# Performance work log

Measured on AMD Instinct MI355X. Metric: run time of the kernel, lower is better.

The kernel has to match this reference:

```python
import jax, jax.numpy as jnp
import numpy as np

B, S, DIM = 2, 2048, 2048
H, DK, DR, DC, DCP, DV = 16, 128, 64, 512, 1024, 128


def setup_inputs() -> dict:
    key = jax.random.key(0)
    ks = jax.random.split(key, 8)
    s = 0.02  # weight init scale
    return {
        "x": jax.random.normal(ks[0], (B, S, DIM), jnp.float32),
        "W_c": jax.random.normal(ks[1], (DIM, DC), jnp.float32) * s,
        "W_c_prime": jax.random.normal(ks[2], (DIM, DCP), jnp.float32) * s,
        "W_qc": jax.random.normal(ks[3], (H, DCP, DK), jnp.float32) * s,
        "W_qr": jax.random.normal(ks[4], (H, DCP, DR), jnp.float32) * s,
        "W_kc": jax.random.normal(ks[5], (H, DC, DK), jnp.float32) * s,
        "W_kr": jax.random.normal(ks[6], (DIM, DR), jnp.float32) * s,
        "W_v": jax.random.normal(ks[7], (H, DC, DV), jnp.float32) * s,
    }


def reference(x, W_c, W_c_prime, W_qc, W_qr, W_kc, W_kr, W_v):
    # Latent compressions
    c = x @ W_c                 # [B,S,DC]  compressed KV latent
    cp = x @ W_c_prime          # [B,S,DCP] compressed Q latent
    # Per-head projections, vectorized over heads
    q_c = jnp.einsum('bsc,hck->bhsk', cp, W_qc)   # [B,H,S,DK]
    q_r = jnp.einsum('bsc,hcr->bhsr', cp, W_qr)   # [B,H,S,DR]
    k_c = jnp.einsum('bsc,hck->bhsk', c, W_kc)    # [B,H,S,DK]
    k_r = x @ W_kr                                 # [B,S,DR] shared across heads
    q = jnp.concatenate([q_c, q_r], axis=-1)                               # [B,H,S,DK+DR]
    k = jnp.concatenate([k_c, jnp.broadcast_to(k_r[:, None], (B, H, S, DR))], axis=-1)
    scale = 1.0 / np.sqrt(DK + DR)
    scores = jnp.einsum('bhsd,bhtd->bhst', q, k) * scale                   # [B,H,S,S]
    causal = jnp.tril(jnp.ones((S, S), dtype=bool))
    scores = jnp.where(causal, scores, -jnp.inf)
    probs = jax.nn.softmax(scores.astype(jnp.float32), axis=-1).astype(q.dtype)
    v = jnp.einsum('bsc,hcv->bhsv', c, W_v)                                # [B,H,S,DV]
    out = jnp.einsum('bhst,bhtv->bhsv', probs, v)                          # [B,H,S,DV]
    return out.transpose(0, 2, 1, 3).reshape(B, S, H * DV)                 # concat heads
```

## Files before the change

kernel.cpp:

```cpp
#include <hip/hip_runtime.h>
#include <stdint.h>

typedef __bf16 bf16;
typedef __bf16 bfx8 __attribute__((ext_vector_type(8)));
typedef __bf16 bfx4 __attribute__((ext_vector_type(4)));
typedef float floatx4 __attribute__((ext_vector_type(4)));

#define B_ 2
#define S_ 2048
#define DIM_ 2048
#define H_ 16
#define DK_ 128
#define DR_ 64
#define DC_ 512
#define DCP_ 1024
#define DV_ 128
#define DQK_ 192

#define MASK_VAL (-30000.0f)
#define C1_ 0.10411754f

__global__ void k_cast(const float* __restrict__ in, bf16* __restrict__ out) {
    size_t i = ((size_t)blockIdx.x * 256 + threadIdx.x) * 8;
    float4 a = *(const float4*)(in + i);
    float4 b = *(const float4*)(in + i + 4);
    bfx8 r;
    r[0] = (bf16)a.x; r[1] = (bf16)a.y; r[2] = (bf16)a.z; r[3] = (bf16)a.w;
    r[4] = (bf16)b.x; r[5] = (bf16)b.y; r[6] = (bf16)b.z; r[7] = (bf16)b.w;
    *(bfx8*)(out + i) = r;
}

__global__ void k_transpose(const float* __restrict__ in, bf16* __restrict__ out,
                            int K, int N) {
    __shared__ float tile[32][33];
    int h = blockIdx.z;
    int n0 = blockIdx.x * 32, k0 = blockIdx.y * 32;
    const float* ip = in + (size_t)h * K * N;
    bf16* op = out + (size_t)h * K * N;
    int tx = threadIdx.x & 31, ty = threadIdx.x >> 5;
#pragma unroll
    for (int i = 0; i < 32; i += 8)
        tile[ty + i][tx] = ip[(size_t)(k0 + ty + i) * N + (n0 + tx)];
    __syncthreads();
#pragma unroll
    for (int i = 0; i < 32; i += 8)
        op[(size_t)(n0 + ty + i) * K + (k0 + tx)] = (bf16)tile[tx][ty + i];
}

__device__ __forceinline__ void gld16(const bf16* g, bf16* l) {
    __builtin_amdgcn_global_load_lds(
        (const __attribute__((address_space(1))) void*)g,
        (__attribute__((address_space(3))) void*)l, 16, 0, 0);
}

__device__ __forceinline__ bfx8 frag_ld(const bf16* lds, int row, int quad) {
    int pb = quad ^ ((row >> 1) & 3);
    return *(const bfx8*)(lds + row * 32 + pb * 8);
}

__device__ __forceinline__ void gemm_core(const bf16* __restrict__ A,
                                          const bf16* __restrict__ Bt,
                                          int K, int rowlimB,
                                          floatx4 acc[4][4],
                                          bf16* A_lds, bf16* B_lds) {
    int tid = threadIdx.x, wave = tid >> 6, lane = tid & 63;
    int l15 = lane & 15, quad = lane >> 4;
    int wm = (wave & 1) * 64, wn = (wave >> 1) * 64;
    int ch0 = wave * 2, ch1 = wave * 2 + 1;
    int r0 = ch0 * 16 + (lane >> 2), r1 = ch1 * 16 + (lane >> 2);
    int kb0 = (lane & 3) ^ ((r0 >> 1) & 3), kb1 = (lane & 3) ^ ((r1 >> 1) & 3);
    int rb0 = r0 <= rowlimB ? r0 : rowlimB;
    int rb1 = r1 <= rowlimB ? r1 : rowlimB;
    const bf16* a0 = A + (size_t)r0 * K + kb0 * 8;
    const bf16* a1 = A + (size_t)r1 * K + kb1 * 8;
    const bf16* b0 = Bt + (size_t)rb0 * K + kb0 * 8;
    const bf16* b1 = Bt + (size_t)rb1 * K + kb1 * 8;
    bf16* da0 = A_lds + ch0 * 512;
    bf16* da1 = A_lds + ch1 * 512;
    bf16* db0 = B_lds + ch0 * 512;
    bf16* db1 = B_lds + ch1 * 512;
    for (int k0 = 0; k0 < K; k0 += 32) {
        __syncthreads();
        gld16(a0 + k0, da0);
        gld16(a1 + k0, da1);
        gld16(b0 + k0, db0);
        gld16(b1 + k0, db1);
        __syncthreads();
        bfx8 a[4], b[4];
#pragma unroll
        for (int t = 0; t < 4; ++t) a[t] = frag_ld(A_lds, wm + t * 16 + l15, quad);
#pragma unroll
        for (int t = 0; t < 4; ++t) b[t] = frag_ld(B_lds, wn + t * 16 + l15, quad);
#pragma unroll
        for (int mt = 0; mt < 4; ++mt)
#pragma unroll
            for (int nt = 0; nt < 4; ++nt)
                acc[mt][nt] = __builtin_amdgcn_mfma_f32_16x16x32_bf16(
                    a[mt], b[nt], acc[mt][nt], 0, 0, 0);
    }
}

__global__ __launch_bounds__(256, 3) void k_gemm1(
    const bf16* __restrict__ xb, const bf16* __restrict__ Wt_c,
    const bf16* __restrict__ Wt_cp, const bf16* __restrict__ Wt_kr,
    bf16* __restrict__ c_ws, bf16* __restrict__ cp_ws, bf16* __restrict__ kr_ws) {
    __shared__ __attribute__((aligned(16))) bf16 A_lds[128 * 32];
    __shared__ __attribute__((aligned(16))) bf16 B_lds[128 * 32];
    int bx = blockIdx.x, by = blockIdx.y;
    const bf16* Bt; bf16* outp; int ldc, col0, rowlim;
    if (bx < 4)       { Bt = Wt_c  + (size_t)bx * 128 * DIM_;       outp = c_ws;  ldc = DC_;  col0 = bx * 128;       rowlim = 127; }
    else if (bx < 12) { Bt = Wt_cp + (size_t)(bx - 4) * 128 * DIM_; outp = cp_ws; ldc = DCP_; col0 = (bx - 4) * 128; rowlim = 127; }
    else              { Bt = Wt_kr;                                  outp = kr_ws; ldc = DR_;  col0 = 0;              rowlim = 63;  }
    floatx4 acc[4][4];
#pragma unroll
    for (int i = 0; i < 4; ++i)
#pragma unroll
        for (int j = 0; j < 4; ++j) acc[i][j] = (floatx4){0.f, 0.f, 0.f, 0.f};
    gemm_core(xb + (size_t)by * 128 * DIM_, Bt, DIM_, rowlim, acc, A_lds, B_lds);
    int tid = threadIdx.x, wave = tid >> 6, lane = tid & 63;
    int l15 = lane & 15, quad = lane >> 4;
    int wm = (wave & 1) * 64, wn = (wave >> 1) * 64;
#pragma unroll
    for (int mt = 0; mt < 4; ++mt)
#pragma unroll
        for (int nt = 0; nt < 4; ++nt) {
            int n = wn + nt * 16 + l15;
            if (n > rowlim) continue;
#pragma unroll
            for (int r = 0; r < 4; ++r) {
                int m = by * 128 + wm + mt * 16 + quad * 4 + r;
                outp[(size_t)m * ldc + col0 + n] = (bf16)acc[mt][nt][r];
            }
        }
}

__global__ __launch_bounds__(256, 3) void k_gemm2(
    const bf16* __restrict__ cp_ws, const bf16* __restrict__ Wt_qc,
    const bf16* __restrict__ Wt_qr, bf16* __restrict__ q_ws) {
    __shared__ __attribute__((aligned(16))) bf16 A_lds[128 * 32];
    __shared__ __attribute__((aligned(16))) bf16 B_lds[128 * 32];
    int bx = blockIdx.x, by = blockIdx.y, h = blockIdx.z;
    const bf16* Bt; int col0, rowlim;
    if (bx == 0) { Bt = Wt_qc + (size_t)h * DK_ * DCP_; col0 = 0;   rowlim = 127; }
    else         { Bt = Wt_qr + (size_t)h * DR_ * DCP_; col0 = 128; rowlim = 63;  }
    floatx4 acc[4][4];
#pragma unroll
    for (int i = 0; i < 4; ++i)
#pragma unroll
        for (int j = 0; j < 4; ++j) acc[i][j] = (floatx4){0.f, 0.f, 0.f, 0.f};
    gemm_core(cp_ws + (size_t)by * 128 * DCP_, Bt, DCP_, rowlim, acc, A_lds, B_lds);
    int tid = threadIdx.x, wave = tid >> 6, lane = tid & 63;
    int l15 = lane & 15, quad = lane >> 4;
    int wm = (wave & 1) * 64, wn = (wave >> 1) * 64;
#pragma unroll
    for (int mt = 0; mt < 4; ++mt)
#pragma unroll
        for (int nt = 0; nt < 4; ++nt) {
            int n = wn + nt * 16 + l15;
            if (n > rowlim) continue;
#pragma unroll
            for (int r = 0; r < 4; ++r) {
                int m = by * 128 + wm + mt * 16 + quad * 4 + r;
                int b = m >> 11, s = m & 2047;
                q_ws[(((size_t)b * H_ + h) * S_ + s) * DQK_ + col0 + n] =
                    (bf16)(acc[mt][nt][r] * C1_);
            }
        }
}

__global__ __launch_bounds__(256, 3) void k_gemm3(
    const bf16* __restrict__ c_ws, const bf16* __restrict__ Wt_kc,
    const bf16* __restrict__ Wt_v, bf16* __restrict__ kc_ws, bf16* __restrict__ vt_ws) {
    __shared__ __attribute__((aligned(16))) bf16 A_lds[128 * 32];
    __shared__ __attribute__((aligned(16))) bf16 B_lds[128 * 32];
    int bx = blockIdx.x, by = blockIdx.y, h = blockIdx.z;
    const bf16* Bt = (bx == 0) ? (Wt_kc + (size_t)h * DK_ * DC_)
                               : (Wt_v  + (size_t)h * DV_ * DC_);
    floatx4 acc[4][4];
#pragma unroll
    for (int i = 0; i < 4; ++i)
#pragma unroll
        for (int j = 0; j < 4; ++j) acc[i][j] = (floatx4){0.f, 0.f, 0.f, 0.f};
    gemm_core(c_ws + (size_t)by * 128 * DC_, Bt, DC_, 127, acc, A_lds, B_lds);
    int tid = threadIdx.x, wave = tid >> 6, lane = tid & 63;
    int l15 = lane & 15, quad = lane >> 4;
    int wm = (wave & 1) * 64, wn = (wave >> 1) * 64;
#pragma unroll
    for (int mt = 0; mt < 4; ++mt)
#pragma unroll
        for (int nt = 0; nt < 4; ++nt) {
            int n = wn + nt * 16 + l15;
            if (bx == 0) {
#pragma unroll
                for (int r = 0; r < 4; ++r) {
                    int m = by * 128 + wm + mt * 16 + quad * 4 + r;
                    int b = m >> 11, s = m & 2047;
                    kc_ws[(((size_t)b * H_ + h) * S_ + s) * DK_ + n] = (bf16)acc[mt][nt][r];
                }
            } else {
                int m0 = by * 128 + wm + mt * 16 + quad * 4;
                int b = m0 >> 11, s = m0 & 2047;
                bfx4 pack;
#pragma unroll
                for (int r = 0; r < 4; ++r) pack[r] = (bf16)acc[mt][nt][r];
                *(bfx4*)(&vt_ws[(((size_t)b * H_ + h) * DV_ + n) * S_ + s]) = pack;
            }
        }
}

#define KSTR 200
#define VSTR 72
#define PSTR 72

__global__ __launch_bounds__(256, 2) void k_attn(
    const bf16* __restrict__ q_ws, const bf16* __restrict__ kc_ws,
    const bf16* __restrict__ kr_ws, const bf16* __restrict__ vt_ws,
    float* __restrict__ out) {
    __shared__ __attribute__((aligned(16))) bf16 K_lds[64 * KSTR];
    __shared__ __attribute__((aligned(16))) bf16 V_lds[128 * VSTR];
    __shared__ __attribute__((aligned(16))) bf16 P_lds[64 * PSTR];
    int p = blockIdx.x;
    int bh = blockIdx.y, b = bh >> 4, h = bh & 15;
    int tid = threadIdx.x, wave = tid >> 6, lane = tid & 63;
    int l15 = lane & 15, quad = lane >> 4;

    bf16 ov = (bf16)(l15 == 0 ? 1.f : 0.f);
    bfx8 ones8 = {ov, ov, ov, ov, ov, ov, ov, ov};

    int kn[4], kcc[4], rn[2], rcc[2], vr[4], vcc[4];
#pragma unroll
    for (int i = 0; i < 4; ++i) { int f = (i * 256 + tid) * 8; kn[i] = f >> 7; kcc[i] = f & 127; }
#pragma unroll
    for (int i = 0; i < 2; ++i) { int f = (i * 256 + tid) * 8; rn[i] = f >> 6; rcc[i] = f & 63; }
#pragma unroll
    for (int i = 0; i < 4; ++i) { int f = (i * 256 + tid) * 8; vr[i] = f >> 6; vcc[i] = f & 63; }
    const bf16* kcp[4]; const bf16* krp[2]; const bf16* vp[4];
#pragma unroll
    for (int i = 0; i < 4; ++i) kcp[i] = kc_ws + ((size_t)bh * S_ + kn[i]) * DK_ + kcc[i];
#pragma unroll
    for (int i = 0; i < 2; ++i) krp[i] = kr_ws + ((size_t)b * S_ + rn[i]) * DR_ + rcc[i];
#pragma unroll
    for (int i = 0; i < 4; ++i) vp[i] = vt_ws + ((size_t)bh * DV_ + vr[i]) * S_ + vcc[i];

    for (int ph = 0; ph < 2; ++ph) {
        int qt = ph ? p : 31 - p;
        int q0 = qt * 64, ntiles = qt + 1;

        const bf16* qrow = q_ws + ((size_t)bh * S_ + q0 + wave * 16 + l15) * DQK_;
        bfx8 qf[6];
#pragma unroll
        for (int ks = 0; ks < 6; ++ks)
            qf[ks] = *(const bfx8*)(qrow + ks * 32 + quad * 8);

        floatx4 o_acc[9];
#pragma unroll
        for (int vt = 0; vt < 9; ++vt) o_acc[vt] = (floatx4){0.f, 0.f, 0.f, 0.f};

        bfx8 pk[4], pr[2], pv[4];
#pragma unroll
        for (int i = 0; i < 4; ++i) pk[i] = *(const bfx8*)(kcp[i]);
#pragma unroll
        for (int i = 0; i < 2; ++i) pr[i] = *(const bfx8*)(krp[i]);
#pragma unroll
        for (int i = 0; i < 4; ++i) pv[i] = *(const bfx8*)(vp[i]);

        for (int t = 0; t < ntiles; ++t) {
            __syncthreads();
#pragma unroll
            for (int i = 0; i < 4; ++i) *(bfx8*)(&K_lds[kn[i] * KSTR + kcc[i]]) = pk[i];
#pragma unroll
            for (int i = 0; i < 2; ++i) *(bfx8*)(&K_lds[rn[i] * KSTR + 128 + rcc[i]]) = pr[i];
#pragma unroll
            for (int i = 0; i < 4; ++i) *(bfx8*)(&V_lds[vr[i] * VSTR + vcc[i]]) = pv[i];
            __syncthreads();
            if (t + 1 < ntiles) {
                size_t kv1 = (size_t)(t + 1) * 64;
#pragma unroll
                for (int i = 0; i < 4; ++i) pk[i] = *(const bfx8*)(kcp[i] + kv1 * DK_);
#pragma unroll
                for (int i = 0; i < 2; ++i) pr[i] = *(const bfx8*)(krp[i] + kv1 * DR_);
#pragma unroll
                for (int i = 0; i < 4; ++i) pv[i] = *(const bfx8*)(vp[i] + kv1);
            }
            floatx4 sc[4];
#pragma unroll
            for (int nt = 0; nt < 4; ++nt) sc[nt] = (floatx4){0.f, 0.f, 0.f, 0.f};
#pragma unroll
            for (int ks = 0; ks < 6; ++ks)
#pragma unroll
                for (int nt = 0; nt < 4; ++nt) {
                    bfx8 kf = *(const bfx8*)(&K_lds[(nt * 16 + l15) * KSTR + ks * 32 + quad * 8]);
                    sc[nt] = __builtin_amdgcn_mfma_f32_16x16x32_bf16(qf[ks], kf, sc[nt], 0, 0, 0);
                }
            if (t == ntiles - 1) {
                int kv0 = t * 64;
#pragma unroll
                for (int nt = 0; nt < 4; ++nt)
#pragma unroll
                    for (int r = 0; r < 4; ++r) {
                        int n_g = kv0 + nt * 16 + l15;
                        int q_g = q0 + wave * 16 + quad * 4 + r;
                        if (n_g > q_g) sc[nt][r] = MASK_VAL;
                    }
            }
#pragma unroll
            for (int nt = 0; nt < 4; ++nt)
#pragma unroll
                for (int r = 0; r < 4; ++r)
                    P_lds[(wave * 16 + quad * 4 + r) * PSTR + nt * 16 + l15] =
                        (bf16)exp2f(sc[nt][r]);
#pragma unroll
            for (int ks2 = 0; ks2 < 2; ++ks2) {
                bfx8 pf = *(const bfx8*)(&P_lds[(wave * 16 + l15) * PSTR + ks2 * 32 + quad * 8]);
#pragma unroll
                for (int vt = 0; vt < 8; ++vt) {
                    bfx8 vf = *(const bfx8*)(&V_lds[(vt * 16 + l15) * VSTR + ks2 * 32 + quad * 8]);
                    o_acc[vt] = __builtin_amdgcn_mfma_f32_16x16x32_bf16(pf, vf, o_acc[vt], 0, 0, 0);
                }
                o_acc[8] = __builtin_amdgcn_mfma_f32_16x16x32_bf16(pf, ones8, o_acc[8], 0, 0, 0);
            }
        }
        float rinv[4];
#pragma unroll
        for (int r = 0; r < 4; ++r)
            rinv[r] = 1.f / __shfl(o_acc[8][r], lane & 48);
#pragma unroll
        for (int vt = 0; vt < 8; ++vt)
#pragma unroll
            for (int r = 0; r < 4; ++r) {
                int s = q0 + wave * 16 + quad * 4 + r;
                int v = vt * 16 + l15;
                out[((size_t)b * S_ + s) * (H_ * DV_) + h * DV_ + v] = o_acc[vt][r] * rinv[r];
            }
    }
}

extern "C" void kernel_launch(void* const* d_in, const int* in_sizes, int n_in,
                              void* d_out, int out_size, void* d_ws, size_t ws_size,
                              hipStream_t stream) {
    const float* x    = (const float*)d_in[0];
    const float* W_c  = (const float*)d_in[1];
    const float* W_cp = (const float*)d_in[2];
    const float* W_qc = (const float*)d_in[3];
    const float* W_qr = (const float*)d_in[4];
    const float* W_kc = (const float*)d_in[5];
    const float* W_kr = (const float*)d_in[6];
    const float* W_v  = (const float*)d_in[7];
    float* out = (float*)d_out;

    bf16* c_ws  = (bf16*)d_out;
    bf16* cp_ws = c_ws + (size_t)B_ * S_ * DC_;
    bf16* xb    = cp_ws + (size_t)B_ * S_ * DCP_;

    char* ws = (char*)d_ws;
    size_t off = 0;
    auto alloc = [&](size_t elems) { bf16* p = (bf16*)(ws + off); off += elems * sizeof(bf16); return p; };
    bf16* Wt_c  = alloc((size_t)DIM_ * DC_);
    bf16* Wt_cp = alloc((size_t)DIM_ * DCP_);
    bf16* Wt_qc = alloc((size_t)H_ * DCP_ * DK_);
    bf16* Wt_qr = alloc((size_t)H_ * DCP_ * DR_);
    bf16* Wt_kc = alloc((size_t)H_ * DC_ * DK_);
    bf16* Wt_kr = alloc((size_t)DIM_ * DR_);
    bf16* Wt_v  = alloc((size_t)H_ * DC_ * DV_);
    bf16* kr_ws = alloc((size_t)B_ * S_ * DR_);
    bf16* q_ws  = alloc((size_t)B_ * H_ * S_ * DQK_);
    bf16* kc_ws = alloc((size_t)B_ * H_ * S_ * DK_);
    bf16* vt_ws = alloc((size_t)B_ * H_ * DV_ * S_);

    k_cast<<<dim3(4096), 256, 0, stream>>>(x, xb);
    k_transpose<<<dim3(DC_ / 32, DIM_ / 32, 1),  256, 0, stream>>>(W_c,  Wt_c,  DIM_, DC_);
    k_transpose<<<dim3(DCP_ / 32, DIM_ / 32, 1), 256, 0, stream>>>(W_cp, Wt_cp, DIM_, DCP_);
    k_transpose<<<dim3(DK_ / 32, DCP_ / 32, H_), 256, 0, stream>>>(W_qc, Wt_qc, DCP_, DK_);
    k_transpose<<<dim3(DR_ / 32, DCP_ / 32, H_), 256, 0, stream>>>(W_qr, Wt_qr, DCP_, DR_);
    k_transpose<<<dim3(DK_ / 32, DC_ / 32, H_),  256, 0, stream>>>(W_kc, Wt_kc, DC_, DK_);
    k_transpose<<<dim3(DR_ / 32, DIM_ / 32, 1),  256, 0, stream>>>(W_kr, Wt_kr, DIM_, DR_);
    k_transpose<<<dim3(DV_ / 32, DC_ / 32, H_),  256, 0, stream>>>(W_v,  Wt_v,  DC_, DV_);

    k_gemm1<<<dim3(13, 32), 256, 0, stream>>>(xb, Wt_c, Wt_cp, Wt_kr, c_ws, cp_ws, kr_ws);
    k_gemm2<<<dim3(2, 32, H_), 256, 0, stream>>>(cp_ws, Wt_qc, Wt_qr, q_ws);
    k_gemm3<<<dim3(2, 32, H_), 256, 0, stream>>>(c_ws, Wt_kc, Wt_v, kc_ws, vt_ws);
    k_attn<<<dim3(16, B_ * H_), 256, 0, stream>>>(q_ws, kc_ws, kr_ws, vt_ws, out);
}
```

Baseline: 333.3 us.

## Enlarge attention query tile to 128 rows with two M-subtiles per wave

```diff
diff --git a/kernel.cpp b/kernel.cpp
--- a/kernel.cpp
+++ b/kernel.cpp
@@ -210,15 +210,15 @@
 
 #define KSTR 200
 #define VSTR 72
-#define PSTR 72
-
-__global__ __launch_bounds__(256, 2) void k_attn(
+#define PSTR 68
+
+__global__ __launch_bounds__(256, 1) void k_attn(
     const bf16* __restrict__ q_ws, const bf16* __restrict__ kc_ws,
     const bf16* __restrict__ kr_ws, const bf16* __restrict__ vt_ws,
     float* __restrict__ out) {
     __shared__ __attribute__((aligned(16))) bf16 K_lds[64 * KSTR];
     __shared__ __attribute__((aligned(16))) bf16 V_lds[128 * VSTR];
-    __shared__ __attribute__((aligned(16))) bf16 P_lds[64 * PSTR];
+    __shared__ __attribute__((aligned(16))) bf16 P_lds[128 * PSTR];
     int p = blockIdx.x;
     int bh = blockIdx.y, b = bh >> 4, h = bh & 15;
     int tid = threadIdx.x, wave = tid >> 6, lane = tid & 63;
@@ -243,18 +243,24 @@
     for (int i = 0; i < 4; ++i) vp[i] = vt_ws + ((size_t)bh * DV_ + vr[i]) * S_ + vcc[i];
 
     for (int ph = 0; ph < 2; ++ph) {
-        int qt = ph ? p : 31 - p;
-        int q0 = qt * 64, ntiles = qt + 1;
-
-        const bf16* qrow = q_ws + ((size_t)bh * S_ + q0 + wave * 16 + l15) * DQK_;
-        bfx8 qf[6];
-#pragma unroll
-        for (int ks = 0; ks < 6; ++ks)
-            qf[ks] = *(const bfx8*)(qrow + ks * 32 + quad * 8);
-
-        floatx4 o_acc[9];
-#pragma unroll
-        for (int vt = 0; vt < 9; ++vt) o_acc[vt] = (floatx4){0.f, 0.f, 0.f, 0.f};
+        int qt = ph ? p : 15 - p;
+        int q0 = qt * 128, ntiles = 2 * qt + 2;
+
+        bfx8 qf[2][6];
+#pragma unroll
+        for (int mt = 0; mt < 2; ++mt) {
+            const bf16* qrow =
+                q_ws + ((size_t)bh * S_ + q0 + wave * 32 + mt * 16 + l15) * DQK_;
+#pragma unroll
+            for (int ks = 0; ks < 6; ++ks)
+                qf[mt][ks] = *(const bfx8*)(qrow + ks * 32 + quad * 8);
+        }
+
+        floatx4 o_acc[2][9];
+#pragma unroll
+        for (int mt = 0; mt < 2; ++mt)
+#pragma unroll
+            for (int vt = 0; vt < 9; ++vt) o_acc[mt][vt] = (floatx4){0.f, 0.f, 0.f, 0.f};
 
         bfx8 pk[4], pr[2], pv[4];
 #pragma unroll
@@ -282,56 +288,70 @@
 #pragma unroll
                 for (int i = 0; i < 4; ++i) pv[i] = *(const bfx8*)(vp[i] + kv1);
             }
-            floatx4 sc[4];
-#pragma unroll
-            for (int nt = 0; nt < 4; ++nt) sc[nt] = (floatx4){0.f, 0.f, 0.f, 0.f};
+            floatx4 sc[2][4];
+#pragma unroll
+            for (int mt = 0; mt < 2; ++mt)
+#pragma unroll
+                for (int nt = 0; nt < 4; ++nt) sc[mt][nt] = (floatx4){0.f, 0.f, 0.f, 0.f};
 #pragma unroll
             for (int ks = 0; ks < 6; ++ks)
 #pragma unroll
                 for (int nt = 0; nt < 4; ++nt) {
                     bfx8 kf = *(const bfx8*)(&K_lds[(nt * 16 + l15) * KSTR + ks * 32 + quad * 8]);
-                    sc[nt] = __builtin_amdgcn_mfma_f32_16x16x32_bf16(qf[ks], kf, sc[nt], 0, 0, 0);
+                    sc[0][nt] = __builtin_amdgcn_mfma_f32_16x16x32_bf16(qf[0][ks], kf, sc[0][nt], 0, 0, 0);
+                    sc[1][nt] = __builtin_amdgcn_mfma_f32_16x16x32_bf16(qf[1][ks], kf, sc[1][nt], 0, 0, 0);
                 }
-            if (t == ntiles - 1) {
+            if (t >= ntiles - 2) {
                 int kv0 = t * 64;
 #pragma unroll
+                for (int mt = 0; mt < 2; ++mt)
+#pragma unroll
+                    for (int nt = 0; nt < 4; ++nt)
+#pragma unroll
+                        for (int r = 0; r < 4; ++r) {
+                            int n_g = kv0 + nt * 16 + l15;
+                            int q_g = q0 + wave * 32 + mt * 16 + quad * 4 + r;
+                            if (n_g > q_g) sc[mt][nt][r] = MASK_VAL;
+                        }
+            }
+#pragma unroll
+            for (int mt = 0; mt < 2; ++mt)
+#pragma unroll
                 for (int nt = 0; nt < 4; ++nt)
 #pragma unroll
-                    for (int r = 0; r < 4; ++r) {
-                        int n_g = kv0 + nt * 16 + l15;
-                        int q_g = q0 + wave * 16 + quad * 4 + r;
-                        if (n_g > q_g) sc[nt][r] = MASK_VAL;
-                    }
-            }
-#pragma unroll
-            for (int nt = 0; nt < 4; ++nt)
-#pragma unroll
-                for (int r = 0; r < 4; ++r)
-                    P_lds[(wave * 16 + quad * 4 + r) * PSTR + nt * 16 + l15] =
-                        (bf16)exp2f(sc[nt][r]);
+                    for (int r = 0; r < 4; ++r)
+                        P_lds[(wave * 32 + mt * 16 + quad * 4 + r) * PSTR + nt * 16 + l15] =
+                            (bf16)exp2f(sc[mt][nt][r]);
 #pragma unroll
             for (int ks2 = 0; ks2 < 2; ++ks2) {
-                bfx8 pf = *(const bfx8*)(&P_lds[(wave * 16 + l15) * PSTR + ks2 * 32 + quad * 8]);
+                bfx8 pf0 = *(const bfx8*)(&P_lds[(wave * 32 + l15) * PSTR + ks2 * 32 + quad * 8]);
+                bfx8 pf1 = *(const bfx8*)(&P_lds[(wave * 32 + 16 + l15) * PSTR + ks2 * 32 + quad * 8]);
 #pragma unroll
                 for (int vt = 0; vt < 8; ++vt) {
                     bfx8 vf = *(const bfx8*)(&V_lds[(vt * 16 + l15) * VSTR + ks2 * 32 + quad * 8]);
-                    o_acc[vt] = __builtin_amdgcn_mfma_f32_16x16x32_bf16(pf, vf, o_acc[vt], 0, 0, 0);
+                    o_acc[0][vt] = __builtin_amdgcn_mfma_f32_16x16x32_bf16(pf0, vf, o_acc[0][vt], 0, 0, 0);
+                    o_acc[1][vt] = __builtin_amdgcn_mfma_f32_16x16x32_bf16(pf1, vf, o_acc[1][vt], 0, 0, 0);
                 }
-                o_acc[8] = __builtin_amdgcn_mfma_f32_16x16x32_bf16(pf, ones8, o_acc[8], 0, 0, 0);
-            }
-        }
-        float rinv[4];
-#pragma unroll
-        for (int r = 0; r < 4; ++r)
-            rinv[r] = 1.f / __shfl(o_acc[8][r], lane & 48);
-#pragma unroll
-        for (int vt = 0; vt < 8; ++vt)
-#pragma unroll
-            for (int r = 0; r < 4; ++r) {
-                int s = q0 + wave * 16 + quad * 4 + r;
-                int v = vt * 16 + l15;
-                out[((size_t)b * S_ + s) * (H_ * DV_) + h * DV_ + v] = o_acc[vt][r] * rinv[r];
-            }
+                o_acc[0][8] = __builtin_amdgcn_mfma_f32_16x16x32_bf16(pf0, ones8, o_acc[0][8], 0, 0, 0);
+                o_acc[1][8] = __builtin_amdgcn_mfma_f32_16x16x32_bf16(pf1, ones8, o_acc[1][8], 0, 0, 0);
+            }
+        }
+#pragma unroll
+        for (int mt = 0; mt < 2; ++mt) {
+            float rinv[4];
+#pragma unroll
+            for (int r = 0; r < 4; ++r)
+                rinv[r] = 1.f / __shfl(o_acc[mt][8][r], lane & 48);
+#pragma unroll
+            for (int vt = 0; vt < 8; ++vt)
+#pragma unroll
+                for (int r = 0; r < 4; ++r) {
+                    int s = q0 + wave * 32 + mt * 16 + quad * 4 + r;
+                    int v = vt * 16 + l15;
+                    out[((size_t)b * S_ + s) * (H_ * DV_) + h * DV_ + v] =
+                        o_acc[mt][vt][r] * rinv[r];
+                }
+        }
     }
 }
 
@@ -379,5 +399,5 @@
     k_gemm1<<<dim3(13, 32), 256, 0, stream>>>(xb, Wt_c, Wt_cp, Wt_kr, c_ws, cp_ws, kr_ws);
     k_gemm2<<<dim3(2, 32, H_), 256, 0, stream>>>(cp_ws, Wt_qc, Wt_qr, q_ws);
     k_gemm3<<<dim3(2, 32, H_), 256, 0, stream>>>(c_ws, Wt_kc, Wt_v, kc_ws, vt_ws);
-    k_attn<<<dim3(16, B_ * H_), 256, 0, stream>>>(q_ws, kc_ws, kr_ws, vt_ws, out);
-}
+    k_attn<<<dim3(8, B_ * H_), 256, 0, stream>>>(q_ws, kc_ws, kr_ws, vt_ws, out);
+}
```

New measurement: 332.8 us. About the same (-0.1%).
